# Kernel tuning notes

Hardware: AMD Instinct MI355X
Metric: run time of the kernel (lower is better)

Reference implementation:

```python
import jax, jax.numpy as jnp
import numpy as np

B, S, D, H = 2, 2048, 1024, 16
DH = D // H


def setup_inputs() -> dict:
    key = jax.random.key(0)
    ks = jax.random.split(key, 12)
    f = lambda k, sh: jax.random.normal(k, sh, dtype=jnp.float32)
    inp = {"q": f(ks[0], (B, S, D)), "k": f(ks[1], (B, S, D)), "v": f(ks[2], (B, S, D))}
    scale = 1.0 / np.sqrt(D)
    names = ["q", "k", "v", "o"]
    for i, n in enumerate(names):
        inp["W" + n] = f(ks[3 + i], (D, D)) * scale
        inp["b" + n] = f(ks[7 + i], (D,)) * scale
    # causal mask: True = masked out
    inp["mask"] = jnp.triu(jnp.ones((S, S), dtype=bool), k=1)[None, None]
    return inp


def _rope(x):
    # x: [b, h, s, dh]; non-standard RoPE from AbsPositionEncoding
    s, dh = x.shape[2], x.shape[3]
    inv = jnp.exp(jnp.arange(0, dh, 2, dtype=jnp.float32) * (-(4.0 * jnp.log(jnp.float32(10.0))) / dh))
    pos = jnp.arange(s, dtype=jnp.float32)[:, None]
    sin = jnp.sin(pos * inv)  # [s, dh/2]
    cos = jnp.cos(pos * inv)
    x1 = x[..., 0::2]
    x2 = x[..., 1::2]
    out = jnp.stack([x1 * sin - x2 * cos, -x1 * cos - x2 * sin], axis=-1)
    return out.reshape(x.shape)


def reference(q, k, v, Wq, bq, Wk, bk, Wv, bv, Wo, bo, mask):
    b, s, d = q.shape
    h, dh = H, DH

    def proj(x, W, bias):
        return (x @ W.T + bias).reshape(b, -1, h, dh).transpose(0, 2, 1, 3)

    Q = proj(q, Wq, bq)
    K = proj(k, Wk, bk)
    V = proj(v, Wv, bv)
    PQ = _rope(Q)
    PK = _rope(K)
    # NOTE: source's forward() path applies NO 1/sqrt(dh) scaling
    scores = jnp.einsum('bhqd,bhkd->bhqk', PQ, PK)
    neg = jnp.finfo(scores.dtype).min
    scores = jnp.where(mask, neg, scores)
    p = jax.nn.softmax(scores, axis=-1)
    p = jnp.where(mask, jnp.float32(0.0), p)
    out = jnp.einsum('bhqk,bhkd->bhqd', p, V)
    out = out.transpose(0, 2, 1, 3).reshape(b, s, d)
    return out @ Wo.T + bo
```

## Files before the change

kernel.cpp:

```cpp
#include <hip/hip_runtime.h>
#include <stdint.h>

#define BB 2
#define SS 2048
#define DD 1024
#define HH 16
#define DH 64
#define MM 4096

typedef __attribute__((ext_vector_type(8))) short short8;
typedef __attribute__((ext_vector_type(4))) float floatx4;
typedef __attribute__((ext_vector_type(16))) float floatx16;
typedef unsigned short u16;

#define MFMA16(a,b,c) __builtin_amdgcn_mfma_f32_16x16x32_bf16((a),(b),(c),0,0,0)
#define MFMA32(a,b,c) __builtin_amdgcn_mfma_f32_32x32x16_bf16((a),(b),(c),0,0,0)

__device__ __forceinline__ u16 f2bf(float f) {
  unsigned u = __float_as_uint(f);
  u += 0x7fffu + ((u >> 16) & 1u);
  return (u16)(u >> 16);
}

__device__ __forceinline__ unsigned cvtpk(float lo, float hi2) {
  unsigned r;
  asm("v_cvt_pk_bf16_f32 %0, %1, %2" : "=v"(r) : "v"(lo), "v"(hi2));
  return r;
}

__device__ __forceinline__ void gll16(const void* g, void* l) {
  __builtin_amdgcn_global_load_lds((const __attribute__((address_space(1))) void*)g,
                                   (__attribute__((address_space(3))) void*)l,
                                   16, 0, 0);
}

__global__ __launch_bounds__(256) void prep(
    const float* __restrict__ q, const float* __restrict__ k, const float* __restrict__ v,
    const float* __restrict__ Wq, const float* __restrict__ Wk,
    const float* __restrict__ Wv, const float* __restrict__ Wo,
    u16* __restrict__ qb, u16* __restrict__ kb, u16* __restrict__ vb,
    u16* __restrict__ wqb, u16* __restrict__ wkb, u16* __restrict__ wvb, u16* __restrict__ wob,
    float2* __restrict__ tab) {
  int bid = blockIdx.x;
  if (bid < 256) {
    const int t = bid * 256 + threadIdx.x;
    const int s = t >> 5, j = t & 31;
    const float inv = expf(-(float)j * (0.125f * 2.302585092994046f));
    const float a = (float)s * inv;
    tab[t] = make_float2(sinf(a), cosf(a));
    return;
  }
  bid -= 256;
  const float* src;
  u16* dst;
  int x;
  if (bid < 12288) {
    const int z = bid >> 12;
    x = bid & 4095;
    src = z == 0 ? q : (z == 1 ? k : v);
    dst = z == 0 ? qb : (z == 1 ? kb : vb);
  } else {
    bid -= 12288;
    const int z = bid >> 10;
    x = bid & 1023;
    src = z == 0 ? Wq : (z == 1 ? Wk : (z == 2 ? Wv : Wo));
    dst = z == 0 ? wqb : (z == 1 ? wkb : (z == 2 ? wvb : wob));
  }
  const int i = (x * 256 + threadIdx.x) * 4;
  const float4 xv = *(const float4*)(src + i);
  ushort4 p; p.x = f2bf(xv.x); p.y = f2bf(xv.y); p.z = f2bf(xv.z); p.w = f2bf(xv.w);
  *(ushort4*)(dst + i) = p;
}

__device__ __forceinline__ void gemm_core128(const u16* __restrict__ A, const u16* __restrict__ Bt,
                                             int K, u16* As, u16* Bs, floatx4 acc[4][4],
                                             int m0, int n0) {
  const int tid = threadIdx.x;
  const int w = tid >> 6, l = tid & 63;
  const int lr = l & 15, lq = l >> 4;
  const int wm = (w >> 1) * 64, wn = (w & 1) * 64;

#pragma unroll
  for (int i = 0; i < 4; ++i)
#pragma unroll
    for (int j = 0; j < 4; ++j) acc[i][j] = (floatx4){0.f, 0.f, 0.f, 0.f};

  const int srow = w * 32 + (l >> 2);
  const int scol = (l & 3) * 8;
  const u16* ag = A + (size_t)(m0 + srow) * K + scol;
  const u16* bg = Bt + (size_t)(n0 + srow) * K + scol;
  u16* as0 = &As[w * 1024];
  u16* bs0 = &Bs[w * 1024];

  for (int k0 = 0; k0 < K; k0 += 32) {
    gll16(ag + k0, as0);
    gll16(ag + (size_t)16 * K + k0, as0 + 512);
    gll16(bg + k0, bs0);
    gll16(bg + (size_t)16 * K + k0, bs0 + 512);
    __syncthreads();
    short8 af[4], bfv[4];
#pragma unroll
    for (int i = 0; i < 4; ++i) af[i] = *(const short8*)&As[(wm + i * 16 + lr) * 32 + lq * 8];
#pragma unroll
    for (int j = 0; j < 4; ++j) bfv[j] = *(const short8*)&Bs[(wn + j * 16 + lr) * 32 + lq * 8];
    __builtin_amdgcn_s_setprio(1);
#pragma unroll
    for (int i = 0; i < 4; ++i)
#pragma unroll
      for (int j = 0; j < 4; ++j) acc[i][j] = MFMA16(af[i], bfv[j], acc[i][j]);
    __builtin_amdgcn_s_setprio(0);
    __syncthreads();
  }
}

__device__ __forceinline__ void gemm_core64(const u16* __restrict__ A, const u16* __restrict__ Bt,
                                            int K, u16* As, u16* Bs, floatx4 acc[2][4],
                                            int m0, int n0) {
  const int tid = threadIdx.x;
  const int w = tid >> 6, l = tid & 63;
  const int lr = l & 15, lq = l >> 4;
  const int wm = (w >> 1) * 32, wn = (w & 1) * 64;

#pragma unroll
  for (int i = 0; i < 2; ++i)
#pragma unroll
    for (int j = 0; j < 4; ++j) acc[i][j] = (floatx4){0.f, 0.f, 0.f, 0.f};

  const int arow = w * 16 + (l >> 2);
  const int brow = w * 32 + (l >> 2);
  const int scol = (l & 3) * 8;
  const u16* ag = A + (size_t)(m0 + arow) * K + scol;
  const u16* bg = Bt + (size_t)(n0 + brow) * K + scol;
  u16* as0 = &As[w * 512];
  u16* bs0 = &Bs[w * 1024];

  for (int k0 = 0; k0 < K; k0 += 32) {
    gll16(ag + k0, as0);
    gll16(bg + k0, bs0);
    gll16(bg + (size_t)16 * K + k0, bs0 + 512);
    __syncthreads();
    short8 af[2], bfv[4];
#pragma unroll
    for (int i = 0; i < 2; ++i) af[i] = *(const short8*)&As[(wm + i * 16 + lr) * 32 + lq * 8];
#pragma unroll
    for (int j = 0; j < 4; ++j) bfv[j] = *(const short8*)&Bs[(wn + j * 16 + lr) * 32 + lq * 8];
    __builtin_amdgcn_s_setprio(1);
#pragma unroll
    for (int i = 0; i < 2; ++i)
#pragma unroll
      for (int j = 0; j < 4; ++j) acc[i][j] = MFMA16(af[i], bfv[j], acc[i][j]);
    __builtin_amdgcn_s_setprio(0);
    __syncthreads();
  }
}

__global__ __launch_bounds__(256) void gemm3_fused(
    const u16* __restrict__ A0, const u16* __restrict__ A1, const u16* __restrict__ A2,
    const u16* __restrict__ B0, const u16* __restrict__ B1, const u16* __restrict__ B2,
    const float* __restrict__ c0, const float* __restrict__ c1, const float* __restrict__ c2,
    u16* __restrict__ Qro, u16* __restrict__ Kro, u16* __restrict__ Vtr,
    const float2* __restrict__ tab) {
  __shared__ alignas(16) u16 As[128 * 32];
  __shared__ alignas(16) u16 Bs[128 * 32];
  const int z = blockIdx.z;
  const u16* A = z == 0 ? A0 : (z == 1 ? A1 : A2);
  const u16* Bt = z == 0 ? B0 : (z == 1 ? B1 : B2);
  const float* bias = z == 0 ? c0 : (z == 1 ? c1 : c2);
  const int m0 = blockIdx.y * 128, n0 = blockIdx.x * 128;

  floatx4 acc[4][4];
  gemm_core128(A, Bt, DD, As, Bs, acc, m0, n0);

  const int tid = threadIdx.x;
  const int w = tid >> 6, l = tid & 63;
  const int lr = l & 15, lq = l >> 4;
  const int wm = (w >> 1) * 64, wn = (w & 1) * 64;

  if (z == 2) {
#pragma unroll
    for (int i = 0; i < 4; ++i) {
      const int row = m0 + wm + i * 16 + lq * 4;
      const int b = row >> 11, s = row & (SS - 1);
#pragma unroll
      for (int j = 0; j < 4; ++j) {
        const int col = n0 + wn + j * 16 + lr;
        const int h = col >> 6, e = col & 63;
        const float bv = bias[col];
        ushort4 pk;
        pk.x = f2bf(acc[i][j][0] + bv);
        pk.y = f2bf(acc[i][j][1] + bv);
        pk.z = f2bf(acc[i][j][2] + bv);
        pk.w = f2bf(acc[i][j][3] + bv);
        *(ushort4*)(Vtr + ((size_t)(b * HH + h) * DH + e) * SS + s) = pk;
      }
    }
  } else {
    u16* dst = z ? Kro : Qro;
#pragma unroll
    for (int i = 0; i < 4; ++i) {
#pragma unroll
      for (int j = 0; j < 4; ++j) {
        const int col = n0 + wn + j * 16 + lr;
        const int h = col >> 6, e = col & 63;
        const float bv = bias[col];
#pragma unroll
        for (int r = 0; r < 4; ++r) {
          const int row = m0 + wm + i * 16 + lq * 4 + r;
          const int b = row >> 11, s = row & (SS - 1);
          const float v = acc[i][j][r] + bv;
          const float p = __shfl_xor(v, 1);
          const float2 sc = tab[s * 32 + (e >> 1)];
          const float ov = ((e & 1) == 0) ? (v * sc.x - p * sc.y)
                                          : (-p * sc.y - v * sc.x);
          dst[((size_t)(b * HH + h) * SS + s) * DH + e] = f2bf(ov);
        }
      }
    }
  }
}

__global__ __launch_bounds__(256) void gemm_bt(const u16* __restrict__ A, const u16* __restrict__ Bt,
                                               const float* __restrict__ bias, float* __restrict__ C,
                                               int M, int N, int K) {
  __shared__ alignas(16) u16 As[64 * 32];
  __shared__ alignas(16) u16 Bs[128 * 32];
  const int m0 = blockIdx.y * 64, n0 = blockIdx.x * 128;
  floatx4 acc[2][4];
  gemm_core64(A, Bt, K, As, Bs, acc, m0, n0);

  const int tid = threadIdx.x;
  const int w = tid >> 6, l = tid & 63;
  const int lr = l & 15, lq = l >> 4;
  const int wm = (w >> 1) * 32, wn = (w & 1) * 64;
#pragma unroll
  for (int i = 0; i < 2; ++i) {
    const int row = m0 + wm + i * 16 + lq * 4;
#pragma unroll
    for (int j = 0; j < 4; ++j) {
      const int col = n0 + wn + j * 16 + lr;
      const float bv = bias[col];
      float* cp = C + (size_t)row * N + col;
#pragma unroll
      for (int r = 0; r < 4; ++r) cp[(size_t)r * N] = acc[i][j][r] + bv;
    }
  }
}

__global__ __launch_bounds__(256) void attn_fwd(const u16* __restrict__ Qr, const u16* __restrict__ Kr,
                                                const u16* __restrict__ Vt, u16* __restrict__ O) {
  __shared__ alignas(16) u16 Ks[2][64 * 64];
  __shared__ alignas(16) u16 Vs[2][64 * 64];
  const int bid = blockIdx.x;
  const int qt = 15 - (bid >> 5);
  const int bh = bid & 31;
  const int w = threadIdx.x >> 6, l = threadIdx.x & 63;
  const int ql = l & 31, hi = l >> 5;
  const int qw0 = qt * 128 + w * 32;
  const u16* Qh = Qr + (size_t)bh * SS * DH;
  const u16* Kh = Kr + (size_t)bh * SS * DH;
  const u16* Vh = Vt + (size_t)bh * DH * SS;

  short8 qf[4];
#pragma unroll
  for (int i = 0; i < 4; ++i)
    qf[i] = *(const short8*)(Qh + (size_t)(qw0 + ql) * DH + i * 16 + hi * 8);

  floatx16 oacc[2];
#pragma unroll
  for (int dt = 0; dt < 2; ++dt)
#pragma unroll
    for (int r = 0; r < 16; ++r) oacc[dt][r] = 0.f;
  float mrun = -1e30f, lrun = 0.f;

  const int srow = w * 16 + (l >> 3);
  const int sgofs = ((((l & 7) * 16) ^ (((l >> 3) & 7) << 4)) >> 1);
  const int swzb = (ql & 7) << 4;

#define STAGE(buf, kv0)                                                                  \
  do {                                                                                   \
    gll16(Kh + (size_t)((kv0) + srow) * DH + sgofs,       &Ks[buf][(w * 16) * 64]);      \
    gll16(Kh + (size_t)((kv0) + srow + 8) * DH + sgofs,   &Ks[buf][(w * 16 + 8) * 64]);  \
    gll16(Vh + (size_t)srow * SS + (kv0) + sgofs,         &Vs[buf][(w * 16) * 64]);      \
    gll16(Vh + (size_t)(srow + 8) * SS + (kv0) + sgofs,   &Vs[buf][(w * 16 + 8) * 64]);  \
  } while (0)

  const int T = 2 * qt + 2;
  STAGE(0, 0);
  __syncthreads();

  for (int t = 0; t < T; ++t) {
    const int cur = t & 1;
    if (t < T - 1) STAGE(cur ^ 1, (t + 1) * 64);
    const int kv0 = t * 64;

    if (kv0 <= qw0 + 31) {
      floatx16 st[2];
#pragma unroll
      for (int tt = 0; tt < 2; ++tt)
#pragma unroll
        for (int r = 0; r < 16; ++r) st[tt][r] = 0.f;
      __builtin_amdgcn_s_setprio(1);
#pragma unroll
      for (int tt = 0; tt < 2; ++tt)
#pragma unroll
        for (int i = 0; i < 4; ++i) {
          const u16* kp = &Ks[cur][(tt * 32 + ql) * 64 + (((32 * i + 16 * hi) ^ swzb) >> 1)];
          st[tt] = MFMA32(*(const short8*)kp, qf[i], st[tt]);
        }
      __builtin_amdgcn_s_setprio(0);

      if (kv0 + 63 > qw0) {
#pragma unroll
        for (int tt = 0; tt < 2; ++tt)
#pragma unroll
          for (int r = 0; r < 16; ++r) {
            const int kv = kv0 + tt * 32 + (r & 3) + 8 * (r >> 2) + 4 * hi;
            if (kv > qw0 + ql) st[tt][r] = -1e30f;
          }
      }

      floatx16 mx;
#pragma unroll
      for (int r = 0; r < 16; ++r) mx[r] = fmaxf(st[0][r], st[1][r]);
      float m8[8];
#pragma unroll
      for (int r = 0; r < 8; ++r) m8[r] = fmaxf(mx[r], mx[r + 8]);
      float m4a = fmaxf(m8[0], m8[4]), m4b = fmaxf(m8[1], m8[5]);
      float m4c = fmaxf(m8[2], m8[6]), m4d = fmaxf(m8[3], m8[7]);
      float tmax = fmaxf(fmaxf(m4a, m4b), fmaxf(m4c, m4d));
      tmax = fmaxf(tmax, __shfl_xor(tmax, 32));

      const float mn = fmaxf(mrun, tmax);
      const float sc = __expf(mrun - mn);
      mrun = mn;
      float ps = 0.f;
#pragma unroll
      for (int tt = 0; tt < 2; ++tt)
#pragma unroll
        for (int r = 0; r < 16; ++r) {
          const float p = __expf(st[tt][r] - mn);
          st[tt][r] = p;
          ps += p;
        }
      ps += __shfl_xor(ps, 32);
      lrun = lrun * sc + ps;
#pragma unroll
      for (int dt = 0; dt < 2; ++dt)
#pragma unroll
        for (int r = 0; r < 16; ++r) oacc[dt][r] *= sc;

      short8 pfrag[4];
#pragma unroll
      for (int c = 0; c < 4; ++c) {
        const int tt = c >> 1;
        const int A0r = 2 * (c & 1), A1r = A0r + 1;
        const unsigned P00 = cvtpk(st[tt][4 * A0r + 0], st[tt][4 * A0r + 1]);
        const unsigned P01 = cvtpk(st[tt][4 * A0r + 2], st[tt][4 * A0r + 3]);
        const unsigned P10 = cvtpk(st[tt][4 * A1r + 0], st[tt][4 * A1r + 1]);
        const unsigned P11 = cvtpk(st[tt][4 * A1r + 2], st[tt][4 * A1r + 3]);
        const unsigned S0 = hi ? P00 : P10;
        const unsigned S1 = hi ? P01 : P11;
        const unsigned R0 = (unsigned)__shfl_xor((int)S0, 32);
        const unsigned R1 = (unsigned)__shfl_xor((int)S1, 32);
        union { unsigned u[4]; short8 s; } fd;
        fd.u[0] = hi ? R0 : P00;
        fd.u[1] = hi ? R1 : P01;
        fd.u[2] = hi ? P10 : R0;
        fd.u[3] = hi ? P11 : R1;
        pfrag[c] = fd.s;
      }

      __builtin_amdgcn_s_setprio(1);
#pragma unroll
      for (int dt = 0; dt < 2; ++dt)
#pragma unroll
        for (int c = 0; c < 4; ++c) {
          const u16* vp = &Vs[cur][(dt * 32 + ql) * 64 + (((32 * c + 16 * hi) ^ swzb) >> 1)];
          oacc[dt] = MFMA32(*(const short8*)vp, pfrag[c], oacc[dt]);
        }
      __builtin_amdgcn_s_setprio(0);
    }
    __syncthreads();
  }
#undef STAGE

  const float inv = 1.0f / lrun;
  const int b = bh >> 4, h = bh & 15;
  u16* orow = O + ((size_t)(b * SS + qw0 + ql)) * DD + h * DH;
#pragma unroll
  for (int dt = 0; dt < 2; ++dt)
#pragma unroll
    for (int g = 0; g < 4; ++g) {
      ushort4 pk;
      pk.x = f2bf(oacc[dt][4 * g + 0] * inv);
      pk.y = f2bf(oacc[dt][4 * g + 1] * inv);
      pk.z = f2bf(oacc[dt][4 * g + 2] * inv);
      pk.w = f2bf(oacc[dt][4 * g + 3] * inv);
      *(ushort4*)(orow + dt * 32 + 8 * g + 4 * hi) = pk;
    }
}

extern "C" void kernel_launch(void* const* d_in, const int* in_sizes, int n_in,
                              void* d_out, int out_size, void* d_ws, size_t ws_size,
                              hipStream_t stream) {
  (void)in_sizes; (void)n_in; (void)out_size; (void)ws_size;
  const float* q  = (const float*)d_in[0];
  const float* k  = (const float*)d_in[1];
  const float* v  = (const float*)d_in[2];
  const float* Wq = (const float*)d_in[3];
  const float* bq = (const float*)d_in[4];
  const float* Wk = (const float*)d_in[5];
  const float* bk = (const float*)d_in[6];
  const float* Wv = (const float*)d_in[7];
  const float* bv = (const float*)d_in[8];
  const float* Wo = (const float*)d_in[9];
  const float* bo = (const float*)d_in[10];
  float* out = (float*)d_out;

  char* ws = (char*)d_ws;
  size_t off = 0;
  auto carve = [&](size_t bytes) { char* p = ws + off; off += (bytes + 255) & ~(size_t)255; return p; };
  u16* qb   = (u16*)carve((size_t)MM * DD * 2);
  u16* kb   = (u16*)carve((size_t)MM * DD * 2);
  u16* vb   = (u16*)carve((size_t)MM * DD * 2);
  u16* wqb  = (u16*)carve((size_t)DD * DD * 2);
  u16* wkb  = (u16*)carve((size_t)DD * DD * 2);
  u16* wvb  = (u16*)carve((size_t)DD * DD * 2);
  u16* wob  = (u16*)carve((size_t)DD * DD * 2);
  u16* Qro  = (u16*)carve((size_t)MM * DD * 2);
  u16* Kro  = (u16*)carve((size_t)MM * DD * 2);
  u16* Vtr  = (u16*)carve((size_t)MM * DD * 2);
  float2* tab = (float2*)carve((size_t)SS * 32 * 8);
  u16* Ob = qb;

  prep<<<256 + 3 * 4096 + 4 * 1024, 256, 0, stream>>>(q, k, v, Wq, Wk, Wv, Wo,
                                                      qb, kb, vb, wqb, wkb, wvb, wob, tab);
  gemm3_fused<<<dim3(DD / 128, MM / 128, 3), 256, 0, stream>>>(qb, kb, vb, wqb, wkb, wvb,
                                                               bq, bk, bv, Qro, Kro, Vtr, tab);
  attn_fwd<<<16 * BB * HH, 256, 0, stream>>>(Qro, Kro, Vtr, Ob);
  gemm_bt<<<dim3(DD / 128, MM / 64), 256, 0, stream>>>(Ob, wob, bo, out, MM, DD, DD);
}
```

Before: 264.0 us.

## Split attention into single-wave blocks with 32-wide KV tiles and no barriers

The attention kernel now launches one 64-thread wavefront per 32-query tile instead of four waves per 128-query tile, with KV processed in 32-column steps. This removes __syncthreads and the wasted work from waves sharing a KV tile past their causal limit, and gives a finer, more balanced grid of 2048 blocks. Waits on vmcnt replace the barriers. In exchange, each wave loads its own K/V tiles, so there is no sharing across waves, more global traffic and more softmax steps per unit of MFMA work.

```diff
diff --git a/kernel.cpp b/kernel.cpp
--- a/kernel.cpp
+++ b/kernel.cpp
@@ -246,16 +246,16 @@
   }
 }
 
-__global__ __launch_bounds__(256) void attn_fwd(const u16* __restrict__ Qr, const u16* __restrict__ Kr,
-                                                const u16* __restrict__ Vt, u16* __restrict__ O) {
-  __shared__ alignas(16) u16 Ks[2][64 * 64];
-  __shared__ alignas(16) u16 Vs[2][64 * 64];
+__global__ __launch_bounds__(64) void attn_fwd(const u16* __restrict__ Qr, const u16* __restrict__ Kr,
+                                               const u16* __restrict__ Vt, u16* __restrict__ O) {
+  __shared__ alignas(16) u16 Ks[2][32 * 64];
+  __shared__ alignas(16) u16 Vs[2][64 * 32];
   const int bid = blockIdx.x;
-  const int qt = 15 - (bid >> 5);
+  const int qi = 63 - (bid >> 5);
   const int bh = bid & 31;
-  const int w = threadIdx.x >> 6, l = threadIdx.x & 63;
+  const int l = threadIdx.x;
   const int ql = l & 31, hi = l >> 5;
-  const int qw0 = qt * 128 + w * 32;
+  const int qw0 = qi * 32;
   const u16* Qh = Qr + (size_t)bh * SS * DH;
   const u16* Kh = Kr + (size_t)bh * SS * DH;
   const u16* Vh = Vt + (size_t)bh * DH * SS;
@@ -272,115 +272,111 @@
     for (int r = 0; r < 16; ++r) oacc[dt][r] = 0.f;
   float mrun = -1e30f, lrun = 0.f;
 
-  const int srow = w * 16 + (l >> 3);
-  const int sgofs = ((((l & 7) * 16) ^ (((l >> 3) & 7) << 4)) >> 1);
-  const int swzb = (ql & 7) << 4;
-
-#define STAGE(buf, kv0)                                                                  \
-  do {                                                                                   \
-    gll16(Kh + (size_t)((kv0) + srow) * DH + sgofs,       &Ks[buf][(w * 16) * 64]);      \
-    gll16(Kh + (size_t)((kv0) + srow + 8) * DH + sgofs,   &Ks[buf][(w * 16 + 8) * 64]);  \
-    gll16(Vh + (size_t)srow * SS + (kv0) + sgofs,         &Vs[buf][(w * 16) * 64]);      \
-    gll16(Vh + (size_t)(srow + 8) * SS + (kv0) + sgofs,   &Vs[buf][(w * 16 + 8) * 64]);  \
+  const int krow = l >> 3;
+  const int kofs = ((((l & 7) * 16) ^ (((l >> 3) & 7) << 4)) >> 1);
+  const int vrow = l >> 2;
+  const int vofs = ((((l & 3) * 16) ^ (((l >> 2) & 3) << 4)) >> 1);
+  const int swzk = (ql & 7) << 4;
+  const int swzv = (ql & 3) << 4;
+
+#define STAGE(buf, kv0)                                                              \
+  do {                                                                               \
+    gll16(Kh + (size_t)((kv0) + krow) * DH + kofs,      &Ks[buf][0 * 64]);           \
+    gll16(Kh + (size_t)((kv0) + krow + 8) * DH + kofs,  &Ks[buf][8 * 64]);           \
+    gll16(Kh + (size_t)((kv0) + krow + 16) * DH + kofs, &Ks[buf][16 * 64]);          \
+    gll16(Kh + (size_t)((kv0) + krow + 24) * DH + kofs, &Ks[buf][24 * 64]);          \
+    gll16(Vh + (size_t)vrow * SS + (kv0) + vofs,        &Vs[buf][0 * 32]);           \
+    gll16(Vh + (size_t)(vrow + 16) * SS + (kv0) + vofs, &Vs[buf][16 * 32]);          \
+    gll16(Vh + (size_t)(vrow + 32) * SS + (kv0) + vofs, &Vs[buf][32 * 32]);          \
+    gll16(Vh + (size_t)(vrow + 48) * SS + (kv0) + vofs, &Vs[buf][48 * 32]);          \
   } while (0)
 
-  const int T = 2 * qt + 2;
+  const int T = qi + 1;
   STAGE(0, 0);
-  __syncthreads();
+  asm volatile("s_waitcnt vmcnt(0)" ::: "memory");
 
   for (int t = 0; t < T; ++t) {
     const int cur = t & 1;
-    if (t < T - 1) STAGE(cur ^ 1, (t + 1) * 64);
-    const int kv0 = t * 64;
-
-    if (kv0 <= qw0 + 31) {
-      floatx16 st[2];
-#pragma unroll
-      for (int tt = 0; tt < 2; ++tt)
-#pragma unroll
-        for (int r = 0; r < 16; ++r) st[tt][r] = 0.f;
-      __builtin_amdgcn_s_setprio(1);
-#pragma unroll
-      for (int tt = 0; tt < 2; ++tt)
-#pragma unroll
-        for (int i = 0; i < 4; ++i) {
-          const u16* kp = &Ks[cur][(tt * 32 + ql) * 64 + (((32 * i + 16 * hi) ^ swzb) >> 1)];
-          st[tt] = MFMA32(*(const short8*)kp, qf[i], st[tt]);
-        }
-      __builtin_amdgcn_s_setprio(0);
-
-      if (kv0 + 63 > qw0) {
-#pragma unroll
-        for (int tt = 0; tt < 2; ++tt)
-#pragma unroll
-          for (int r = 0; r < 16; ++r) {
-            const int kv = kv0 + tt * 32 + (r & 3) + 8 * (r >> 2) + 4 * hi;
-            if (kv > qw0 + ql) st[tt][r] = -1e30f;
-          }
+    if (t < T - 1) {
+      STAGE(cur ^ 1, (t + 1) * 32);
+      asm volatile("s_waitcnt vmcnt(8)" ::: "memory");
+    } else {
+      asm volatile("s_waitcnt vmcnt(0)" ::: "memory");
+    }
+
+    floatx16 st;
+#pragma unroll
+    for (int r = 0; r < 16; ++r) st[r] = 0.f;
+    __builtin_amdgcn_s_setprio(1);
+#pragma unroll
+    for (int i = 0; i < 4; ++i) {
+      const u16* kp = &Ks[cur][ql * 64 + (((32 * i + 16 * hi) ^ swzk) >> 1)];
+      st = MFMA32(*(const short8*)kp, qf[i], st);
+    }
+    __builtin_amdgcn_s_setprio(0);
+
+    if (t == T - 1) {
+#pragma unroll
+      for (int r = 0; r < 16; ++r) {
+        const int kv = (r & 3) + 8 * (r >> 2) + 4 * hi;
+        if (kv > ql) st[r] = -1e30f;
       }
-
-      floatx16 mx;
-#pragma unroll
-      for (int r = 0; r < 16; ++r) mx[r] = fmaxf(st[0][r], st[1][r]);
-      float m8[8];
-#pragma unroll
-      for (int r = 0; r < 8; ++r) m8[r] = fmaxf(mx[r], mx[r + 8]);
-      float m4a = fmaxf(m8[0], m8[4]), m4b = fmaxf(m8[1], m8[5]);
-      float m4c = fmaxf(m8[2], m8[6]), m4d = fmaxf(m8[3], m8[7]);
-      float tmax = fmaxf(fmaxf(m4a, m4b), fmaxf(m4c, m4d));
-      tmax = fmaxf(tmax, __shfl_xor(tmax, 32));
-
-      const float mn = fmaxf(mrun, tmax);
-      const float sc = __expf(mrun - mn);
-      mrun = mn;
-      float ps = 0.f;
-#pragma unroll
-      for (int tt = 0; tt < 2; ++tt)
-#pragma unroll
-        for (int r = 0; r < 16; ++r) {
-          const float p = __expf(st[tt][r] - mn);
-          st[tt][r] = p;
-          ps += p;
-        }
-      ps += __shfl_xor(ps, 32);
-      lrun = lrun * sc + ps;
-#pragma unroll
-      for (int dt = 0; dt < 2; ++dt)
-#pragma unroll
-        for (int r = 0; r < 16; ++r) oacc[dt][r] *= sc;
-
-      short8 pfrag[4];
-#pragma unroll
-      for (int c = 0; c < 4; ++c) {
-        const int tt = c >> 1;
-        const int A0r = 2 * (c & 1), A1r = A0r + 1;
-        const unsigned P00 = cvtpk(st[tt][4 * A0r + 0], st[tt][4 * A0r + 1]);
-        const unsigned P01 = cvtpk(st[tt][4 * A0r + 2], st[tt][4 * A0r + 3]);
-        const unsigned P10 = cvtpk(st[tt][4 * A1r + 0], st[tt][4 * A1r + 1]);
-        const unsigned P11 = cvtpk(st[tt][4 * A1r + 2], st[tt][4 * A1r + 3]);
-        const unsigned S0 = hi ? P00 : P10;
-        const unsigned S1 = hi ? P01 : P11;
-        const unsigned R0 = (unsigned)__shfl_xor((int)S0, 32);
-        const unsigned R1 = (unsigned)__shfl_xor((int)S1, 32);
-        union { unsigned u[4]; short8 s; } fd;
-        fd.u[0] = hi ? R0 : P00;
-        fd.u[1] = hi ? R1 : P01;
-        fd.u[2] = hi ? P10 : R0;
-        fd.u[3] = hi ? P11 : R1;
-        pfrag[c] = fd.s;
+    }
+
+    float m8[8];
+#pragma unroll
+    for (int r = 0; r < 8; ++r) m8[r] = fmaxf(st[r], st[r + 8]);
+    float m4a = fmaxf(m8[0], m8[4]), m4b = fmaxf(m8[1], m8[5]);
+    float m4c = fmaxf(m8[2], m8[6]), m4d = fmaxf(m8[3], m8[7]);
+    float tmax = fmaxf(fmaxf(m4a, m4b), fmaxf(m4c, m4d));
+    tmax = fmaxf(tmax, __shfl_xor(tmax, 32));
+
+    const float mn = fmaxf(mrun, tmax);
+    const float sc = __expf(mrun - mn);
+    mrun = mn;
+    float ps = 0.f;
+#pragma unroll
+    for (int r = 0; r < 16; ++r) {
+      const float p = __expf(st[r] - mn);
+      st[r] = p;
+      ps += p;
+    }
+    ps += __shfl_xor(ps, 32);
+    lrun = lrun * sc + ps;
+#pragma unroll
+    for (int dt = 0; dt < 2; ++dt)
+#pragma unroll
+      for (int r = 0; r < 16; ++r) oacc[dt][r] *= sc;
+
+    short8 pfrag[2];
+#pragma unroll
+    for (int c = 0; c < 2; ++c) {
+      const int A0r = 2 * c, A1r = A0r + 1;
+      const unsigned P00 = cvtpk(st[4 * A0r + 0], st[4 * A0r + 1]);
+      const unsigned P01 = cvtpk(st[4 * A0r + 2], st[4 * A0r + 3]);
+      const unsigned P10 = cvtpk(st[4 * A1r + 0], st[4 * A1r + 1]);
+      const unsigned P11 = cvtpk(st[4 * A1r + 2], st[4 * A1r + 3]);
+      const unsigned S0 = hi ? P00 : P10;
+      const unsigned S1 = hi ? P01 : P11;
+      const unsigned R0 = (unsigned)__shfl_xor((int)S0, 32);
+      const unsigned R1 = (unsigned)__shfl_xor((int)S1, 32);
+      union { unsigned u[4]; short8 s; } fd;
+      fd.u[0] = hi ? R0 : P00;
+      fd.u[1] = hi ? R1 : P01;
+      fd.u[2] = hi ? P10 : R0;
+      fd.u[3] = hi ? P11 : R1;
+      pfrag[c] = fd.s;
+    }
+
+    __builtin_amdgcn_s_setprio(1);
+#pragma unroll
+    for (int dt = 0; dt < 2; ++dt)
+#pragma unroll
+      for (int c = 0; c < 2; ++c) {
+        const u16* vp = &Vs[cur][(dt * 32 + ql) * 32 + (((32 * c + 16 * hi) ^ swzv) >> 1)];
+        oacc[dt] = MFMA32(*(const short8*)vp, pfrag[c], oacc[dt]);
       }
-
-      __builtin_amdgcn_s_setprio(1);
-#pragma unroll
-      for (int dt = 0; dt < 2; ++dt)
-#pragma unroll
-        for (int c = 0; c < 4; ++c) {
-          const u16* vp = &Vs[cur][(dt * 32 + ql) * 64 + (((32 * c + 16 * hi) ^ swzb) >> 1)];
-          oacc[dt] = MFMA32(*(const short8*)vp, pfrag[c], oacc[dt]);
-        }
-      __builtin_amdgcn_s_setprio(0);
-    }
-    __syncthreads();
+    __builtin_amdgcn_s_setprio(0);
   }
 #undef STAGE
 
@@ -437,6 +433,6 @@
                                                       qb, kb, vb, wqb, wkb, wvb, wob, tab);
   gemm3_fused<<<dim3(DD / 128, MM / 128, 3), 256, 0, stream>>>(qb, kb, vb, wqb, wkb, wvb,
                                                                bq, bk, bv, Qro, Kro, Vtr, tab);
-  attn_fwd<<<16 * BB * HH, 256, 0, stream>>>(Qro, Kro, Vtr, Ob);
+  attn_fwd<<<64 * BB * HH, 64, 0, stream>>>(Qro, Kro, Vtr, Ob);
   gemm_bt<<<dim3(DD / 128, MM / 64), 256, 0, stream>>>(Ob, wob, bo, out, MM, DD, DD);
 }
```

After: 280.4 us. 1.06x slower.
